# Kernel optimization log

Measured on AMD Instinct MI355X. Metric: run time of the kernel, lower is better.

## Reference

```python
import jax, jax.numpy as jnp
import numpy as np

ENC_DIM = 256
DEC_DIM = 256
INT_DIM = 256


def setup_inputs() -> dict:
    key = jax.random.key(0)
    k1, k2, k3, k4, k5 = jax.random.split(key, 5)
    B, T = 64, 2048
    encoder_states = jax.random.normal(k1, (B, T, ENC_DIM), dtype=jnp.float32)
    decoder_state = jax.random.normal(k2, (B, DEC_DIM), dtype=jnp.float32)
    s1 = 1.0 / np.sqrt(ENC_DIM)
    s2 = 1.0 / np.sqrt(DEC_DIM)
    s3 = 1.0 / np.sqrt(INT_DIM)
    w1 = jax.random.uniform(k3, (INT_DIM, ENC_DIM), jnp.float32, -s1, s1)
    w2 = jax.random.uniform(k4, (INT_DIM, DEC_DIM), jnp.float32, -s2, s2)
    v = jax.random.uniform(k5, (1, INT_DIM), jnp.float32, -s3, s3)
    return {"encoder_states": encoder_states, "decoder_state": decoder_state,
            "w1": w1, "w2": w2, "v": v}


def reference(encoder_states, decoder_state, w1, w2, v):
    # scores: v @ tanh(W1 e_t + W2 d) for all t at once
    enc_proj = jnp.einsum('bte,ie->bti', encoder_states, w1)      # [B,T,I]
    dec_proj = jnp.einsum('bd,id->bi', decoder_state, w2)          # [B,I]
    scores = jnp.einsum('bti,oi->bt', jnp.tanh(enc_proj + dec_proj[:, None, :]), v)  # [B,T]
    attention_probs = jax.nn.softmax(scores, axis=1)[:, :, None]   # [B,T,1]
    final_context_vec = jnp.sum(attention_probs * encoder_states, axis=1)  # [B,E]
    return final_context_vec, attention_probs
```

## Files before the change

kernel.cpp:

```cpp
#include <hip/hip_runtime.h>
#include <hip/hip_bf16.h>
#include <math.h>

#define Bq 64
#define Tq 2048
#define Eq 256
#define Dq 256
#define Iq 256

using short8  = __attribute__((ext_vector_type(8))) short;
using floatx4 = __attribute__((ext_vector_type(4))) float;

__device__ __forceinline__ float fast_tanh(float x) {
    float e = __expf(2.0f * x);
    return 1.0f - 2.0f / (e + 1.0f);
}

__device__ __forceinline__ ushort f2bf(float x) {
    union { __hip_bfloat16 h; ushort u; } c;
    c.h = __float2bfloat16(x);
    return c.u;
}

__global__ __launch_bounds__(256) void prep_kernel(
    const float* __restrict__ w1, ushort* __restrict__ w1sw,
    const float* __restrict__ dec, const float* __restrict__ w2,
    float* __restrict__ dproj)
{
    if (blockIdx.x < 32) {
        const int kc = blockIdx.x;
        const int i  = threadIdx.x;
        const float* src = w1 + i * Eq + kc * 8;
        float4 f0 = *(const float4*)src;
        float4 f1 = *(const float4*)(src + 4);
        ushort u[8] = { f2bf(f0.x), f2bf(f0.y), f2bf(f0.z), f2bf(f0.w),
                        f2bf(f1.x), f2bf(f1.y), f2bf(f1.z), f2bf(f1.w) };
        *(short8*)&w1sw[(kc * 256 + i) * 8] = *(short8*)u;
    } else {
        const int b = blockIdx.x - 32;
        const int i = threadIdx.x;
        __shared__ float dls[Dq];
        dls[i] = dec[b * Dq + i];
        __syncthreads();
        const float* w2r = w2 + i * Dq;
        float acc = 0.f;
        #pragma unroll 8
        for (int d = 0; d < Dq; ++d) acc += dls[d] * w2r[d];
        dproj[b * Iq + i] = acc;
    }
}

__global__ __launch_bounds__(256) void scores_ctx_kernel(
    const float*  __restrict__ enc,
    const ushort* __restrict__ w1sw,
    const float*  __restrict__ v,
    const float*  __restrict__ dproj,
    float* __restrict__ escore,
    float* __restrict__ ctxp,
    float* __restrict__ denomp)
{
    const int b   = blockIdx.y;
    const int bx  = blockIdx.x;
    const int t0  = bx * 64;
    const int tid = threadIdx.x;
    const int w   = tid >> 6;
    const int l   = tid & 63;
    const int l15 = l & 15;
    const int lq  = l >> 4;

    __shared__ alignas(16) ushort As[2][64 * 72];
    __shared__ float vls[Iq], dls[Iq];
    __shared__ float pv[64];
    __shared__ float swred[4 * 64];

    vls[tid] = v[tid];
    dls[tid] = dproj[b * Iq + tid];

    floatx4 acc[4][4];
    #pragma unroll
    for (int mi = 0; mi < 4; ++mi)
        #pragma unroll
        for (int ni = 0; ni < 4; ++ni)
            acc[mi][ni] = (floatx4)0.f;

    const float* encB = enc + ((size_t)b * Tq + t0) * Eq;

    const int srow = tid >> 4;
    const int sc4  = (tid & 15) * 4;

    {
        float4 st[4];
        #pragma unroll
        for (int r = 0; r < 4; ++r)
            st[r] = *(const float4*)&encB[(srow + 16 * r) * Eq + sc4];
        #pragma unroll
        for (int r = 0; r < 4; ++r) {
            ushort4 u;
            u.x = f2bf(st[r].x); u.y = f2bf(st[r].y);
            u.z = f2bf(st[r].z); u.w = f2bf(st[r].w);
            *(ushort4*)&As[0][(srow + 16 * r) * 72 + sc4] = u;
        }
    }
    __syncthreads();

    const ushort* w1b = w1sw + (w * 64 + l15) * 8;

    #pragma unroll
    for (int k0i = 0; k0i < 4; ++k0i) {
        const int cur = k0i & 1;

        short8 bfv[2][4];
        #pragma unroll
        for (int ks = 0; ks < 2; ++ks) {
            const int kc = k0i * 8 + ks * 4 + lq;
            #pragma unroll
            for (int ni = 0; ni < 4; ++ni)
                bfv[ks][ni] = *(const short8*)&w1b[((size_t)kc * 256 + ni * 16) * 8];
        }

        float4 st[4];
        if (k0i < 3) {
            #pragma unroll
            for (int r = 0; r < 4; ++r)
                st[r] = *(const float4*)&encB[(srow + 16 * r) * Eq + (k0i * 64 + 64) + sc4];
        }

        __builtin_amdgcn_s_setprio(1);
        #pragma unroll
        for (int ks = 0; ks < 2; ++ks) {
            const int kloc = ks * 32 + lq * 8;
            short8 af[4];
            #pragma unroll
            for (int mi = 0; mi < 4; ++mi)
                af[mi] = *(const short8*)&As[cur][(mi * 16 + l15) * 72 + kloc];
            #pragma unroll
            for (int mi = 0; mi < 4; ++mi)
                #pragma unroll
                for (int ni = 0; ni < 4; ++ni)
                    acc[mi][ni] = __builtin_amdgcn_mfma_f32_16x16x32_bf16(
                        af[mi], bfv[ks][ni], acc[mi][ni], 0, 0, 0);
        }
        __builtin_amdgcn_s_setprio(0);

        if (k0i < 3) {
            #pragma unroll
            for (int r = 0; r < 4; ++r) {
                ushort4 u;
                u.x = f2bf(st[r].x); u.y = f2bf(st[r].y);
                u.z = f2bf(st[r].z); u.w = f2bf(st[r].w);
                *(ushort4*)&As[cur ^ 1][(srow + 16 * r) * 72 + sc4] = u;
            }
            __syncthreads();
        }
    }

    float part[4][4];
    #pragma unroll
    for (int mi = 0; mi < 4; ++mi)
        #pragma unroll
        for (int r = 0; r < 4; ++r) part[mi][r] = 0.f;

    #pragma unroll
    for (int ni = 0; ni < 4; ++ni) {
        const int i    = w * 64 + ni * 16 + l15;
        const float vi = vls[i];
        const float dp = dls[i];
        #pragma unroll
        for (int mi = 0; mi < 4; ++mi)
            #pragma unroll
            for (int r = 0; r < 4; ++r)
                part[mi][r] += vi * fast_tanh(acc[mi][ni][r] + dp);
    }

    #pragma unroll
    for (int mi = 0; mi < 4; ++mi)
        #pragma unroll
        for (int r = 0; r < 4; ++r) {
            float x = part[mi][r];
            x += __shfl_xor(x, 1); x += __shfl_xor(x, 2);
            x += __shfl_xor(x, 4); x += __shfl_xor(x, 8);
            part[mi][r] = x;
        }
    if (l15 == 0) {
        #pragma unroll
        for (int mi = 0; mi < 4; ++mi)
            #pragma unroll
            for (int r = 0; r < 4; ++r)
                swred[w * 64 + mi * 16 + lq * 4 + r] = part[mi][r];
    }
    __syncthreads();

    if (tid < 64) {
        float s = swred[tid] + swred[64 + tid] + swred[128 + tid] + swred[192 + tid];
        const float es = __expf(s);
        pv[tid] = es;
        escore[(size_t)b * Tq + t0 + tid] = es;
        float tot = es;
        tot += __shfl_xor(tot, 1);  tot += __shfl_xor(tot, 2);
        tot += __shfl_xor(tot, 4);  tot += __shfl_xor(tot, 8);
        tot += __shfl_xor(tot, 16); tot += __shfl_xor(tot, 32);
        if (tid == 0) denomp[bx * Bq + b] = tot;
    }
    __syncthreads();

    const int tg = tid >> 6;
    const int el = (tid & 63) * 4;
    float4 a = {0.f, 0.f, 0.f, 0.f};
    #pragma unroll 8
    for (int tt = 0; tt < 16; ++tt) {
        const int t = tg * 16 + tt;
        const float pt = pv[t];
        float4 ev = *(const float4*)&encB[t * Eq + el];
        a.x += pt * ev.x; a.y += pt * ev.y; a.z += pt * ev.z; a.w += pt * ev.w;
    }
    float* redf = (float*)&As[0][0];
    *(float4*)&redf[tg * 256 + el] = a;
    __syncthreads();
    if (tg == 0) {
        float4 a0 = *(const float4*)&redf[0 * 256 + el];
        float4 a1 = *(const float4*)&redf[1 * 256 + el];
        float4 a2 = *(const float4*)&redf[2 * 256 + el];
        float4 a3 = *(const float4*)&redf[3 * 256 + el];
        float4 o;
        o.x = a0.x + a1.x + a2.x + a3.x;
        o.y = a0.y + a1.y + a2.y + a3.y;
        o.z = a0.z + a1.z + a2.z + a3.z;
        o.w = a0.w + a1.w + a2.w + a3.w;
        *(float4*)&ctxp[((size_t)bx * Bq + b) * Eq + el] = o;
    }
}

__global__ __launch_bounds__(256) void finalize_kernel(
    const float* __restrict__ ctxp, const float* __restrict__ denomp,
    float* __restrict__ probs, float* __restrict__ ctx)
{
    const int b   = blockIdx.x;
    const int tid = threadIdx.x;

    float d = denomp[(tid & 31) * Bq + b];
    d += __shfl_xor(d, 1);  d += __shfl_xor(d, 2);  d += __shfl_xor(d, 4);
    d += __shfl_xor(d, 8);  d += __shfl_xor(d, 16);
    const float inv = 1.0f / d;

    float* prow = probs + (size_t)b * Tq + tid * 8;
    float4 p0 = *(const float4*)(prow + 0);
    float4 p1 = *(const float4*)(prow + 4);
    p0.x *= inv; p0.y *= inv; p0.z *= inv; p0.w *= inv;
    p1.x *= inv; p1.y *= inv; p1.z *= inv; p1.w *= inv;
    *(float4*)(prow + 0) = p0;
    *(float4*)(prow + 4) = p1;

    float s = 0.f;
    #pragma unroll 8
    for (int c = 0; c < 32; ++c)
        s += ctxp[((size_t)c * Bq + b) * Eq + tid];
    ctx[b * Eq + tid] = s * inv;
}

extern "C" void kernel_launch(void* const* d_in, const int* in_sizes, int n_in,
                              void* d_out, int out_size, void* d_ws, size_t ws_size,
                              hipStream_t stream) {
    const float* enc = (const float*)d_in[0];
    const float* dec = (const float*)d_in[1];
    const float* w1  = (const float*)d_in[2];
    const float* w2  = (const float*)d_in[3];
    const float* v   = (const float*)d_in[4];

    float* out   = (float*)d_out;
    float* ctx   = out;
    float* probs = out + Bq * Eq;

    char* ws = (char*)d_ws;
    float*  ctxp   = (float*)ws;
    float*  denomp = (float*)(ws + (32*Bq*Eq)*4);
    float*  dproj  = (float*)(ws + (32*Bq*Eq)*4 + 32*Bq*4);
    ushort* w1sw   = (ushort*)(ws + (32*Bq*Eq)*4 + 32*Bq*4 + Bq*Iq*4);

    prep_kernel<<<dim3(96), dim3(256), 0, stream>>>(w1, w1sw, dec, w2, dproj);
    scores_ctx_kernel<<<dim3(Tq / 64, Bq), dim3(256), 0, stream>>>(
        enc, w1sw, v, dproj, probs, ctxp, denomp);
    finalize_kernel<<<dim3(Bq), dim3(256), 0, stream>>>(ctxp, denomp, probs, ctx);
}
```

Baseline: 224.5 us.

## Stage encoder tiles via async global-to-LDS loads with XOR swizzle

Replaces the register-staged fp32-to-bf16 conversion of encoder tiles with direct global_load_lds async copies of raw fp32 into a swizzled shared buffer. Conversion to bf16 now happens when fragments are read from LDS, and the next tile's load is issued before the current tile's MFMAs. It also sets launch bounds for 4 blocks per CU, vectorizes the dproj dot product, uses a fast reciprocal in tanh, and broadcasts softmax weights with shuffles instead of shared memory. In exchange, LDS usage doubles (fp32 tiles) and every wave repeats the bf16 conversion.

```diff
diff --git a/kernel.cpp b/kernel.cpp
--- a/kernel.cpp
+++ b/kernel.cpp
@@ -13,13 +13,19 @@
 
 __device__ __forceinline__ float fast_tanh(float x) {
     float e = __expf(2.0f * x);
-    return 1.0f - 2.0f / (e + 1.0f);
+    return fmaf(-2.0f, __builtin_amdgcn_rcpf(e + 1.0f), 1.0f);
 }
 
 __device__ __forceinline__ ushort f2bf(float x) {
     union { __hip_bfloat16 h; ushort u; } c;
     c.h = __float2bfloat16(x);
     return c.u;
+}
+
+__device__ __forceinline__ void async_load16(const void* g, void* l) {
+    __builtin_amdgcn_global_load_lds(
+        (const __attribute__((address_space(1))) void*)g,
+        (__attribute__((address_space(3))) void*)l, 16, 0, 0);
 }
 
 __global__ __launch_bounds__(256) void prep_kernel(
@@ -45,12 +51,16 @@
         const float* w2r = w2 + i * Dq;
         float acc = 0.f;
         #pragma unroll 8
-        for (int d = 0; d < Dq; ++d) acc += dls[d] * w2r[d];
+        for (int d = 0; d < Dq; d += 4) {
+            float4 wv = *(const float4*)&w2r[d];
+            float4 dv = *(const float4*)&dls[d];
+            acc += wv.x * dv.x + wv.y * dv.y + wv.z * dv.z + wv.w * dv.w;
+        }
         dproj[b * Iq + i] = acc;
     }
 }
 
-__global__ __launch_bounds__(256) void scores_ctx_kernel(
+__global__ __launch_bounds__(256, 4) void scores_ctx_kernel(
     const float*  __restrict__ enc,
     const ushort* __restrict__ w1sw,
     const float*  __restrict__ v,
@@ -68,9 +78,8 @@
     const int l15 = l & 15;
     const int lq  = l >> 4;
 
-    __shared__ alignas(16) ushort As[2][64 * 72];
+    __shared__ alignas(16) float Af[2][64 * 64];
     __shared__ float vls[Iq], dls[Iq];
-    __shared__ float pv[64];
     __shared__ float swred[4 * 64];
 
     vls[tid] = v[tid];
@@ -85,73 +94,56 @@
 
     const float* encB = enc + ((size_t)b * Tq + t0) * Eq;
 
-    const int srow = tid >> 4;
-    const int sc4  = (tid & 15) * 4;
-
-    {
-        float4 st[4];
-        #pragma unroll
-        for (int r = 0; r < 4; ++r)
-            st[r] = *(const float4*)&encB[(srow + 16 * r) * Eq + sc4];
-        #pragma unroll
-        for (int r = 0; r < 4; ++r) {
-            ushort4 u;
-            u.x = f2bf(st[r].x); u.y = f2bf(st[r].y);
-            u.z = f2bf(st[r].z); u.w = f2bf(st[r].w);
-            *(ushort4*)&As[0][(srow + 16 * r) * 72 + sc4] = u;
-        }
-    }
+    const int rS = w * 4 + lq;
+    const int cS = l15 ^ rS;
+    #define STAGE(kt, buf)                                                   \
+        _Pragma("unroll")                                                    \
+        for (int q = 0; q < 4; ++q) {                                        \
+            const int r = q * 16 + rS;                                       \
+            async_load16(encB + (size_t)r * Eq + (kt) * 64 + cS * 4,         \
+                         &Af[buf][(q * 256 + w * 64) * 4]);                  \
+        }
+
+    STAGE(0, 0);
     __syncthreads();
 
-    const ushort* w1b = w1sw + (w * 64 + l15) * 8;
+    const ushort* vb = w1sw + ((w * 64 + l15) * 8 + lq * 2048);
 
     #pragma unroll
     for (int k0i = 0; k0i < 4; ++k0i) {
         const int cur = k0i & 1;
-
-        short8 bfv[2][4];
+        if (k0i < 3) { STAGE(k0i + 1, cur ^ 1); }
+
         #pragma unroll
         for (int ks = 0; ks < 2; ++ks) {
-            const int kc = k0i * 8 + ks * 4 + lq;
+            short8 bfv[4];
             #pragma unroll
             for (int ni = 0; ni < 4; ++ni)
-                bfv[ks][ni] = *(const short8*)&w1b[((size_t)kc * 256 + ni * 16) * 8];
-        }
-
-        float4 st[4];
-        if (k0i < 3) {
-            #pragma unroll
-            for (int r = 0; r < 4; ++r)
-                st[r] = *(const float4*)&encB[(srow + 16 * r) * Eq + (k0i * 64 + 64) + sc4];
-        }
-
-        __builtin_amdgcn_s_setprio(1);
-        #pragma unroll
-        for (int ks = 0; ks < 2; ++ks) {
-            const int kloc = ks * 32 + lq * 8;
+                bfv[ni] = *(const short8*)(vb + (k0i * 8 + ks * 4) * 2048 + ni * 128);
+
             short8 af[4];
             #pragma unroll
-            for (int mi = 0; mi < 4; ++mi)
-                af[mi] = *(const short8*)&As[cur][(mi * 16 + l15) * 72 + kloc];
+            for (int mi = 0; mi < 4; ++mi) {
+                const int rr = mi * 16 + l15;
+                const int s0 = (ks * 8 + lq * 2) ^ l15;
+                const int s1 = s0 ^ 1;
+                float4 f0 = *(const float4*)&Af[cur][rr * 64 + s0 * 4];
+                float4 f1 = *(const float4*)&Af[cur][rr * 64 + s1 * 4];
+                ushort u[8] = { f2bf(f0.x), f2bf(f0.y), f2bf(f0.z), f2bf(f0.w),
+                                f2bf(f1.x), f2bf(f1.y), f2bf(f1.z), f2bf(f1.w) };
+                af[mi] = *(short8*)u;
+            }
+
+            __builtin_amdgcn_s_setprio(1);
             #pragma unroll
             for (int mi = 0; mi < 4; ++mi)
                 #pragma unroll
                 for (int ni = 0; ni < 4; ++ni)
                     acc[mi][ni] = __builtin_amdgcn_mfma_f32_16x16x32_bf16(
-                        af[mi], bfv[ks][ni], acc[mi][ni], 0, 0, 0);
-        }
-        __builtin_amdgcn_s_setprio(0);
-
-        if (k0i < 3) {
-            #pragma unroll
-            for (int r = 0; r < 4; ++r) {
-                ushort4 u;
-                u.x = f2bf(st[r].x); u.y = f2bf(st[r].y);
-                u.z = f2bf(st[r].z); u.w = f2bf(st[r].w);
-                *(ushort4*)&As[cur ^ 1][(srow + 16 * r) * 72 + sc4] = u;
-            }
-            __syncthreads();
-        }
+                        af[mi], bfv[ni], acc[mi][ni], 0, 0, 0);
+            __builtin_amdgcn_s_setprio(0);
+        }
+        if (k0i < 3) __syncthreads();
     }
 
     float part[4][4];
@@ -190,33 +182,30 @@
     }
     __syncthreads();
 
-    if (tid < 64) {
-        float s = swred[tid] + swred[64 + tid] + swred[128 + tid] + swred[192 + tid];
-        const float es = __expf(s);
-        pv[tid] = es;
-        escore[(size_t)b * Tq + t0 + tid] = es;
+    float s = swred[l] + swred[64 + l] + swred[128 + l] + swred[192 + l];
+    const float es = __expf(s);
+    if (w == 0) {
+        escore[(size_t)b * Tq + t0 + l] = es;
         float tot = es;
         tot += __shfl_xor(tot, 1);  tot += __shfl_xor(tot, 2);
         tot += __shfl_xor(tot, 4);  tot += __shfl_xor(tot, 8);
         tot += __shfl_xor(tot, 16); tot += __shfl_xor(tot, 32);
-        if (tid == 0) denomp[bx * Bq + b] = tot;
-    }
-    __syncthreads();
-
-    const int tg = tid >> 6;
-    const int el = (tid & 63) * 4;
+        if (l == 0) denomp[bx * Bq + b] = tot;
+    }
+
+    const int el = l * 4;
     float4 a = {0.f, 0.f, 0.f, 0.f};
     #pragma unroll 8
     for (int tt = 0; tt < 16; ++tt) {
-        const int t = tg * 16 + tt;
-        const float pt = pv[t];
+        const int t = w * 16 + tt;
+        const float pt = __shfl(es, t);
         float4 ev = *(const float4*)&encB[t * Eq + el];
         a.x += pt * ev.x; a.y += pt * ev.y; a.z += pt * ev.z; a.w += pt * ev.w;
     }
-    float* redf = (float*)&As[0][0];
-    *(float4*)&redf[tg * 256 + el] = a;
+    float* redf = (float*)&Af[0][0];
+    *(float4*)&redf[w * 256 + el] = a;
     __syncthreads();
-    if (tg == 0) {
+    if (w == 0) {
         float4 a0 = *(const float4*)&redf[0 * 256 + el];
         float4 a1 = *(const float4*)&redf[1 * 256 + el];
         float4 a2 = *(const float4*)&redf[2 * 256 + el];
```

Measured after the change: 225.9 us. About the same (+0.6%).
